# Performance work log

Hardware: AMD Instinct MI355X
Metric: run time of the kernel (lower is better)

## Reference

```python
import jax, jax.numpy as jnp
import numpy as np

B, S, I, C, P = 64, 14, 32, 10, 4   # batch, spatial, in-caps/pos, classes, pose size
ROUTINGS = 3
EPS = 1e-9


def setup_inputs() -> dict:
    key = jax.random.key(0)
    k1, k2, k3, k4, k5 = jax.random.split(key, 5)
    return {
        "inputs_pose": jax.random.normal(k1, (B, S, S, I, P, P), jnp.float32),
        "inputs_activation": jax.random.uniform(k2, (B, S, S, I), jnp.float32),
        "w": jax.random.normal(k3, (1, I, C, P, P), jnp.float32),
        "beta_v": jax.random.normal(k4, (1, C), jnp.float32) * 0.1,
        "beta_a": jax.random.normal(k5, (1, C), jnp.float32) * 0.1,
    }


def _em_routing(votes, i_act, beta_v, beta_a, routings):
    # votes: [B, N, C, 16], i_act: [B, N]
    Bn, N, Cc, D = votes.shape
    rr = jnp.full((Bn, N, Cc, 1), 1.0 / Cc, votes.dtype)  # uniform init assignments
    bv = beta_v.reshape(1, 1, Cc, 1)
    ba = beta_a.reshape(1, 1, Cc, 1)
    it_min, it_max = 1.0, min(float(routings), 3.0)  # inverse-temperature schedule
    o_mean = o_act = None
    for it in range(routings):
        inv_temp = it_min + (it_max - it_min) * it / max(1.0, routings - 1.0)
        # --- M step ---
        rr_p = rr * i_act[:, :, None, None]                        # [B,N,C,1]
        rr_sum = jnp.sum(rr_p, axis=1, keepdims=True)              # [B,1,C,1]
        o_mean = jnp.sum(rr_p * votes, axis=1, keepdims=True) / rr_sum   # [B,1,C,16]
        o_var = jnp.sum(rr_p * jnp.square(votes - o_mean), axis=1, keepdims=True) / rr_sum
        o_stdv = jnp.sqrt(o_var)                                   # [B,1,C,16]
        cost = jnp.sum((bv + jnp.log(o_stdv + EPS)) * rr_sum, axis=-1, keepdims=True)  # [B,1,C,1]
        o_act = jax.nn.sigmoid(inv_temp * (ba - cost))             # [B,1,C,1]
        # --- E step (skipped on last iteration) ---
        if it < routings - 1:
            logp = (-jnp.sum(jnp.square(votes - o_mean) / (2.0 * jnp.square(o_stdv) + EPS),
                             axis=-1, keepdims=True)
                    - jnp.sum(jnp.log(o_stdv + EPS), axis=-1, keepdims=True))  # [B,N,C,1]
            zz = jnp.log(o_act + EPS) + logp
            rr = jax.nn.softmax(zz, axis=2)
    return o_mean[:, 0], o_act[:, 0, :, 0]  # [B,C,16], [B,C]


def reference(inputs_pose, inputs_activation, w, beta_v, beta_a):
    # mat_transform: votes[b,h,w,i,c] = pose[b,h,w,i] @ W[i,c]   (4x4 matmuls)
    votes = jnp.einsum('bhwipq,icqr->bhwicpr', inputs_pose, w[0])
    votes = votes.reshape(B, S, S, I, C, P * P)
    # coordinate addition: scaled (row+0.5)/S onto pose element 0, col onto element 1
    coord = (jnp.arange(S, dtype=votes.dtype) + 0.5) / S
    votes = votes.at[..., 0].add(coord[None, :, None, None, None])
    votes = votes.at[..., 1].add(coord[None, None, :, None, None])
    votes = votes.reshape(B, S * S * I, C, P * P)
    acts = inputs_activation.reshape(B, S * S * I)
    o_mean, o_act = _em_routing(votes, acts, beta_v, beta_a, ROUTINGS)
    pose = o_mean.reshape(B, C, P, P)
    return pose, o_act
```

## Files before the change

### kernel.cpp

```cpp
#include <hip/hip_runtime.h>
#include <math.h>

#define Bsz 64
#define Ssz 14
#define Isz 32
#define Csz 10
#define Psz 4
#define Dsz 16
#define Nsz (Ssz*Ssz*Isz)
#define EPSF 1e-9f

__global__ __launch_bounds__(256) void m_step_kernel(
    const float* __restrict__ pose,
    const float* __restrict__ act,
    const float* __restrict__ w,
    const float* __restrict__ beta_v,
    const float* __restrict__ beta_a,
    const float* __restrict__ rr_p,
    float* __restrict__ params,
    float* __restrict__ out,
    float inv_temp, int uniform, int final_it)
{
    const int bc = blockIdx.x;
    const int b = bc / Csz, c = bc % Csz;
    const int tid = threadIdx.x;

    __shared__ float Wc[Isz*17];
    __shared__ float red[4][33];

    for (int t = tid; t < Isz*Dsz; t += 256) {
        int i = t >> 4, qr = t & 15;
        Wc[i*17 + qr] = w[(i*Csz + c)*Dsz + qr];
    }
    __syncthreads();

    float s0 = 0.f;
    float s1[Dsz], s2[Dsz];
#pragma unroll
    for (int d = 0; d < Dsz; ++d) { s1[d] = 0.f; s2[d] = 0.f; }

    const float* poseb = pose + (size_t)b * Nsz * Dsz;
    const float* actb  = act  + (size_t)b * Nsz;
    const float* rrb   = rr_p + ((size_t)b * Csz + c) * Nsz;

    for (int n = tid; n < Nsz; n += 256) {
        const float4* pp = reinterpret_cast<const float4*>(poseb + (size_t)n * Dsz);
        float4 a0 = pp[0], a1 = pp[1], a2 = pp[2], a3 = pp[3];
        float p[16] = {a0.x,a0.y,a0.z,a0.w, a1.x,a1.y,a1.z,a1.w,
                       a2.x,a2.y,a2.z,a2.w, a3.x,a3.y,a3.z,a3.w};
        int i  = n & (Isz-1);
        int hw = n >> 5;
        int wcol = hw % Ssz, hrow = hw / Ssz;
        float wgt = uniform ? (actb[n] * (1.0f/Csz)) : rrb[n];

        const float* Wi = &Wc[i*17];
        float v[16];
#pragma unroll
        for (int pr = 0; pr < 4; ++pr) {
#pragma unroll
            for (int r = 0; r < 4; ++r) {
                v[pr*4+r] = p[pr*4+0]*Wi[0*4+r] + p[pr*4+1]*Wi[1*4+r]
                          + p[pr*4+2]*Wi[2*4+r] + p[pr*4+3]*Wi[3*4+r];
            }
        }
        v[0] += (hrow + 0.5f) * (1.0f/Ssz);
        v[1] += (wcol + 0.5f) * (1.0f/Ssz);

        s0 += wgt;
#pragma unroll
        for (int d = 0; d < Dsz; ++d) {
            float wv = wgt * v[d];
            s1[d] += wv;
            s2[d] += wv * v[d];
        }
    }

#pragma unroll
    for (int m = 32; m >= 1; m >>= 1) {
        s0 += __shfl_xor(s0, m);
#pragma unroll
        for (int d = 0; d < Dsz; ++d) {
            s1[d] += __shfl_xor(s1[d], m);
            s2[d] += __shfl_xor(s2[d], m);
        }
    }
    const int wave = tid >> 6, lane = tid & 63;
    if (lane == 0) {
        red[wave][0] = s0;
#pragma unroll
        for (int d = 0; d < Dsz; ++d) { red[wave][1+d] = s1[d]; red[wave][17+d] = s2[d]; }
    }
    __syncthreads();

    if (tid == 0) {
        float S0 = red[0][0] + red[1][0] + red[2][0] + red[3][0];
        float sumlog = 0.f;
        float mean[16], invd[16];
#pragma unroll
        for (int d = 0; d < Dsz; ++d) {
            float S1 = red[0][1+d]  + red[1][1+d]  + red[2][1+d]  + red[3][1+d];
            float S2 = red[0][17+d] + red[1][17+d] + red[2][17+d] + red[3][17+d];
            float mn  = S1 / S0;
            float var = fmaxf(S2 / S0 - mn*mn, 0.f);
            float stdv = sqrtf(var);
            sumlog += logf(stdv + EPSF);
            mean[d] = mn;
            invd[d] = 1.f / (2.f*var + EPSF);
        }
        float cost = S0 * (16.f * beta_v[c] + sumlog);
        float oact = 1.f / (1.f + expf(-inv_temp * (beta_a[c] - cost)));

        float* prm = params + (size_t)(b*Csz + c) * 33;
#pragma unroll
        for (int d = 0; d < Dsz; ++d) { prm[d] = mean[d]; prm[16+d] = invd[d]; }
        prm[32] = logf(oact + EPSF) - sumlog;

        if (final_it) {
            float* om = out + (size_t)(b*Csz + c) * Dsz;
#pragma unroll
            for (int d = 0; d < Dsz; ++d) om[d] = mean[d];
            out[Bsz*Csz*Dsz + b*Csz + c] = oact;
        }
    }
}

__global__ __launch_bounds__(256) void e_step_kernel(
    const float* __restrict__ pose,
    const float* __restrict__ act,
    const float* __restrict__ w,
    const float* __restrict__ params,
    float* __restrict__ rr_p)
{
    const int b = blockIdx.y;
    const int tid = threadIdx.x;
    const int n = blockIdx.x * 256 + tid;

    __shared__ float Wl[Isz*161];
    __shared__ float prm[Csz*33];

    for (int t = tid; t < Isz*Csz*Dsz; t += 256) {
        int i = t / (Csz*Dsz);
        int rest = t - i*(Csz*Dsz);
        Wl[i*161 + rest] = w[t];
    }
    for (int t = tid; t < Csz*33; t += 256)
        prm[t] = params[(size_t)b*Csz*33 + t];
    __syncthreads();

    if (n >= Nsz) return;

    const float4* pp = reinterpret_cast<const float4*>(pose + ((size_t)b * Nsz + n) * Dsz);
    float4 a0 = pp[0], a1 = pp[1], a2 = pp[2], a3 = pp[3];
    float p[16] = {a0.x,a0.y,a0.z,a0.w, a1.x,a1.y,a1.z,a1.w,
                   a2.x,a2.y,a2.z,a2.w, a3.x,a3.y,a3.z,a3.w};
    float a = act[(size_t)b*Nsz + n];
    const int i = n & (Isz-1);
    const int hw = n >> 5;
    const int wcol = hw % Ssz, hrow = hw / Ssz;
    const float ch = (hrow + 0.5f) * (1.0f/Ssz);
    const float cw = (wcol + 0.5f) * (1.0f/Ssz);

    float zz[Csz];
#pragma unroll
    for (int c = 0; c < Csz; ++c) {
        const float* Wi = &Wl[i*161 + c*16];
        const float* pc = &prm[c*33];
        float quad = 0.f;
#pragma unroll
        for (int pr = 0; pr < 4; ++pr) {
#pragma unroll
            for (int r = 0; r < 4; ++r) {
                float v = p[pr*4+0]*Wi[0*4+r] + p[pr*4+1]*Wi[1*4+r]
                        + p[pr*4+2]*Wi[2*4+r] + p[pr*4+3]*Wi[3*4+r];
                const int d = pr*4 + r;
                if (d == 0) v += ch;
                if (d == 1) v += cw;
                float dv = v - pc[d];
                quad += dv * dv * pc[16+d];
            }
        }
        zz[c] = pc[32] - quad;
    }

    float zmax = zz[0];
#pragma unroll
    for (int c = 1; c < Csz; ++c) zmax = fmaxf(zmax, zz[c]);
    float zsum = 0.f;
#pragma unroll
    for (int c = 0; c < Csz; ++c) { zz[c] = expf(zz[c] - zmax); zsum += zz[c]; }
    const float sc = a / zsum;
#pragma unroll
    for (int c = 0; c < Csz; ++c)
        rr_p[((size_t)b*Csz + c)*Nsz + n] = zz[c] * sc;
}

extern "C" void kernel_launch(void* const* d_in, const int* in_sizes, int n_in,
                              void* d_out, int out_size, void* d_ws, size_t ws_size,
                              hipStream_t stream)
{
    const float* pose = (const float*)d_in[0];
    const float* act  = (const float*)d_in[1];
    const float* w    = (const float*)d_in[2];
    const float* bv   = (const float*)d_in[3];
    const float* ba   = (const float*)d_in[4];
    float* out = (float*)d_out;

    float* rr_p   = (float*)d_ws;
    float* params = rr_p + (size_t)Bsz*Csz*Nsz;

    dim3 egrid((Nsz + 255)/256, Bsz);

    m_step_kernel<<<Bsz*Csz, 256, 0, stream>>>(pose, act, w, bv, ba, rr_p, params, out, 1.0f, 1, 0);
    e_step_kernel<<<egrid, 256, 0, stream>>>(pose, act, w, params, rr_p);
    m_step_kernel<<<Bsz*Csz, 256, 0, stream>>>(pose, act, w, bv, ba, rr_p, params, out, 2.0f, 0, 0);
    e_step_kernel<<<egrid, 256, 0, stream>>>(pose, act, w, params, rr_p);
    m_step_kernel<<<Bsz*Csz, 256, 0, stream>>>(pose, act, w, bv, ba, rr_p, params, out, 3.0f, 0, 1);
}
```

Baseline: 237.2 us.

## Split M-step reduction over N chunks with separate finalize kernel

The M-step reduction for each (batch, class) pair is split across 8 chunks of the N dimension, so eight times more blocks are launched. Each block writes 33 partial sums to a workspace, and a new small finalize kernel combines them and computes the mean, variance, activation and E-step parameters. This is meant to raise GPU occupancy and shorten each block's serial loop. The cost is repeated per-block shared-memory W loads and shuffle reductions, plus an extra kernel launch per iteration.

```diff
diff --git a/kernel.cpp b/kernel.cpp
--- a/kernel.cpp
+++ b/kernel.cpp
@@ -10,18 +10,19 @@
 #define Nsz (Ssz*Ssz*Isz)
 #define EPSF 1e-9f
 
-__global__ __launch_bounds__(256) void m_step_kernel(
+#define NCH 8
+#define CHUNK 784
+
+__global__ __launch_bounds__(256) void m_partial_kernel(
     const float* __restrict__ pose,
     const float* __restrict__ act,
     const float* __restrict__ w,
-    const float* __restrict__ beta_v,
-    const float* __restrict__ beta_a,
     const float* __restrict__ rr_p,
-    float* __restrict__ params,
-    float* __restrict__ out,
-    float inv_temp, int uniform, int final_it)
+    float* __restrict__ partials,
+    int uniform)
 {
     const int bc = blockIdx.x;
+    const int chunk = blockIdx.y;
     const int b = bc / Csz, c = bc % Csz;
     const int tid = threadIdx.x;
 
@@ -43,7 +44,8 @@
     const float* actb  = act  + (size_t)b * Nsz;
     const float* rrb   = rr_p + ((size_t)b * Csz + c) * Nsz;
 
-    for (int n = tid; n < Nsz; n += 256) {
+    const int n_end = chunk*CHUNK + CHUNK;
+    for (int n = chunk*CHUNK + tid; n < n_end; n += 256) {
         const float4* pp = reinterpret_cast<const float4*>(poseb + (size_t)n * Dsz);
         float4 a0 = pp[0], a1 = pp[1], a2 = pp[2], a3 = pp[3];
         float p[16] = {a0.x,a0.y,a0.z,a0.w, a1.x,a1.y,a1.z,a1.w,
@@ -92,35 +94,58 @@
     }
     __syncthreads();
 
-    if (tid == 0) {
-        float S0 = red[0][0] + red[1][0] + red[2][0] + red[3][0];
-        float sumlog = 0.f;
-        float mean[16], invd[16];
-#pragma unroll
-        for (int d = 0; d < Dsz; ++d) {
-            float S1 = red[0][1+d]  + red[1][1+d]  + red[2][1+d]  + red[3][1+d];
-            float S2 = red[0][17+d] + red[1][17+d] + red[2][17+d] + red[3][17+d];
-            float mn  = S1 / S0;
-            float var = fmaxf(S2 / S0 - mn*mn, 0.f);
-            float stdv = sqrtf(var);
-            sumlog += logf(stdv + EPSF);
-            mean[d] = mn;
-            invd[d] = 1.f / (2.f*var + EPSF);
-        }
-        float cost = S0 * (16.f * beta_v[c] + sumlog);
-        float oact = 1.f / (1.f + expf(-inv_temp * (beta_a[c] - cost)));
-
-        float* prm = params + (size_t)(b*Csz + c) * 33;
-#pragma unroll
-        for (int d = 0; d < Dsz; ++d) { prm[d] = mean[d]; prm[16+d] = invd[d]; }
-        prm[32] = logf(oact + EPSF) - sumlog;
-
-        if (final_it) {
-            float* om = out + (size_t)(b*Csz + c) * Dsz;
-#pragma unroll
-            for (int d = 0; d < Dsz; ++d) om[d] = mean[d];
-            out[Bsz*Csz*Dsz + b*Csz + c] = oact;
-        }
+    if (tid < 33) {
+        float v4 = red[0][tid] + red[1][tid] + red[2][tid] + red[3][tid];
+        partials[((size_t)bc*NCH + chunk)*33 + tid] = v4;
+    }
+}
+
+__global__ __launch_bounds__(64) void m_finalize_kernel(
+    const float* __restrict__ partials,
+    const float* __restrict__ beta_v,
+    const float* __restrict__ beta_a,
+    float* __restrict__ params,
+    float* __restrict__ out,
+    float inv_temp, int final_it)
+{
+    const int bc = blockIdx.x * 64 + threadIdx.x;
+    if (bc >= Bsz*Csz) return;
+    const int b = bc / Csz, c = bc % Csz;
+
+    float S[33];
+#pragma unroll
+    for (int j = 0; j < 33; ++j) S[j] = 0.f;
+    const float* pb = partials + (size_t)bc * NCH * 33;
+    for (int ch = 0; ch < NCH; ++ch)
+#pragma unroll
+        for (int j = 0; j < 33; ++j) S[j] += pb[ch*33 + j];
+
+    float S0 = S[0];
+    float sumlog = 0.f;
+    float mean[16], invd[16];
+#pragma unroll
+    for (int d = 0; d < Dsz; ++d) {
+        float S1 = S[1+d], S2 = S[17+d];
+        float mn  = S1 / S0;
+        float var = fmaxf(S2 / S0 - mn*mn, 0.f);
+        float stdv = sqrtf(var);
+        sumlog += logf(stdv + EPSF);
+        mean[d] = mn;
+        invd[d] = 1.f / (2.f*var + EPSF);
+    }
+    float cost = S0 * (16.f * beta_v[c] + sumlog);
+    float oact = 1.f / (1.f + expf(-inv_temp * (beta_a[c] - cost)));
+
+    float* prm = params + (size_t)bc * 33;
+#pragma unroll
+    for (int d = 0; d < Dsz; ++d) { prm[d] = mean[d]; prm[16+d] = invd[d]; }
+    prm[32] = logf(oact + EPSF) - sumlog;
+
+    if (final_it) {
+        float* om = out + (size_t)bc * Dsz;
+#pragma unroll
+        for (int d = 0; d < Dsz; ++d) om[d] = mean[d];
+        out[Bsz*Csz*Dsz + bc] = oact;
     }
 }
 
@@ -205,14 +230,20 @@
     const float* ba   = (const float*)d_in[4];
     float* out = (float*)d_out;
 
-    float* rr_p   = (float*)d_ws;
-    float* params = rr_p + (size_t)Bsz*Csz*Nsz;
-
+    float* rr_p     = (float*)d_ws;
+    float* partials = rr_p + (size_t)Bsz*Csz*Nsz;
+    float* params   = partials + (size_t)Bsz*Csz*NCH*33;
+
+    dim3 mgrid(Bsz*Csz, NCH);
     dim3 egrid((Nsz + 255)/256, Bsz);
-
-    m_step_kernel<<<Bsz*Csz, 256, 0, stream>>>(pose, act, w, bv, ba, rr_p, params, out, 1.0f, 1, 0);
+    dim3 fgrid((Bsz*Csz + 63)/64);
+
+    m_partial_kernel<<<mgrid, 256, 0, stream>>>(pose, act, w, rr_p, partials, 1);
+    m_finalize_kernel<<<fgrid, 64, 0, stream>>>(partials, bv, ba, params, out, 1.0f, 0);
     e_step_kernel<<<egrid, 256, 0, stream>>>(pose, act, w, params, rr_p);
-    m_step_kernel<<<Bsz*Csz, 256, 0, stream>>>(pose, act, w, bv, ba, rr_p, params, out, 2.0f, 0, 0);
+    m_partial_kernel<<<mgrid, 256, 0, stream>>>(pose, act, w, rr_p, partials, 0);
+    m_finalize_kernel<<<fgrid, 64, 0, stream>>>(partials, bv, ba, params, out, 2.0f, 0);
     e_step_kernel<<<egrid, 256, 0, stream>>>(pose, act, w, params, rr_p);
-    m_step_kernel<<<Bsz*Csz, 256, 0, stream>>>(pose, act, w, bv, ba, rr_p, params, out, 3.0f, 0, 1);
-}
+    m_partial_kernel<<<mgrid, 256, 0, stream>>>(pose, act, w, rr_p, partials, 0);
+    m_finalize_kernel<<<fgrid, 64, 0, stream>>>(partials, bv, ba, params, out, 3.0f, 1);
+}
```

After: 307.5 us. 29.6% more time.
